# Optimization experiments

Measured on AMD Instinct MI355X. Metric: run time of the kernel, lower is better.

## Reference

```python
import jax, jax.numpy as jnp
import numpy as np


def setup_inputs() -> dict:
    key = jax.random.key(0)
    k1, k2, k3 = jax.random.split(key, 3)
    B, C, N, Ht, Wt = 2, 16, 512, 64, 64
    Ho, Wo = 1024, 1024
    x = jax.random.normal(k1, (B, C, N, Ht, Wt), dtype=jnp.float32)
    quad_idx = jax.random.randint(k2, (Ho, Wo), 0, N, dtype=jnp.int64)
    tex_uv = jax.random.uniform(k3, (Ho, Wo, 2), dtype=jnp.float32)
    return {"x": x, "quad_idx": quad_idx, "tex_uv": tex_uv}


def reference(x, quad_idx, tex_uv):
    """Per-pixel texture gather + bilinear UV sampling.

    x:        [B, C, N, Ht, Wt] atlas of N textures
    quad_idx: [Ho, Wo] int texture index per output pixel
    tex_uv:   [Ho, Wo, 2] normalized (u, v) in [0, 1]
    returns:  [B, C, Ho, Wo]
    """
    B, C, N, Ht, Wt = x.shape
    Ho, Wo = quad_idx.shape

    # map normalized uv -> pixel coordinates
    u = tex_uv[..., 0] * (Wt - 1)  # [Ho, Wo]
    v = tex_uv[..., 1] * (Ht - 1)

    x0f = jnp.floor(u)
    y0f = jnp.floor(v)
    wu = u - x0f  # bilinear weights
    wv = v - y0f

    x0 = jnp.clip(x0f.astype(jnp.int32), 0, Wt - 1)
    y0 = jnp.clip(y0f.astype(jnp.int32), 0, Ht - 1)
    x1 = jnp.clip(x0 + 1, 0, Wt - 1)
    y1 = jnp.clip(y0 + 1, 0, Ht - 1)

    # flatten texture atlas so one gather covers (texture, y, x)
    flat = x.reshape(B, C, N * Ht * Wt)
    base = quad_idx.astype(jnp.int32) * (Ht * Wt)  # [Ho, Wo]

    def gather(yi, xi):
        idx = (base + yi * Wt + xi).reshape(-1)            # [Ho*Wo]
        return jnp.take(flat, idx, axis=2).reshape(B, C, Ho, Wo)

    g00 = gather(y0, x0)
    g01 = gather(y0, x1)
    g10 = gather(y1, x0)
    g11 = gather(y1, x1)

    wu = wu[None, None]  # [1, 1, Ho, Wo]
    wv = wv[None, None]
    out = ((1.0 - wv) * ((1.0 - wu) * g00 + wu * g01)
           + wv * ((1.0 - wu) * g10 + wu * g11))
    return out
```

## Files before the change

kernel.cpp:

```cpp
#include <hip/hip_runtime.h>

#define HT 64
#define WT 64
#define NTEX 512
#define HO 1024
#define WO 1024
#define NCH 32
#define SLAB (HT * WT)
#define NPIX (HO * WO)

typedef float    f32x4 __attribute__((ext_vector_type(4)));
typedef unsigned u32x4 __attribute__((ext_vector_type(4)));

#define WS_BASE   0
#define WS_CURSOR 4096
#define WS_T1     16384
#define MB (1u << 20)
#define WS_NEED_SMALL ((size_t)WS_T1 + 8 * (size_t)MB)
#define WS_NEED_BIG   ((size_t)WS_T1 + 140 * (size_t)MB)

#define HB_PIX 4096
__global__ __launch_bounds__(256) void k_hist(const int* __restrict__ qi,
                                              unsigned* __restrict__ hist) {
    __shared__ unsigned h[NTEX];
    for (int i = threadIdx.x; i < NTEX; i += 256) h[i] = 0;
    __syncthreads();
    const int p0 = blockIdx.x * HB_PIX;
    for (int k = threadIdx.x; k < HB_PIX; k += 256)
        atomicAdd(&h[qi[p0 + k]], 1u);
    __syncthreads();
    for (int i = threadIdx.x; i < NTEX; i += 256) {
        unsigned v = h[i];
        if (v) atomicAdd(&hist[i << 4], v);
    }
}

__global__ __launch_bounds__(512) void k_scan(const unsigned* __restrict__ hist,
                                              unsigned* __restrict__ base,
                                              unsigned* __restrict__ cursor) {
    __shared__ unsigned t[NTEX];
    const int i = threadIdx.x;
    const unsigned h = hist[i << 4];
    t[i] = h;
    __syncthreads();
    for (int s = 1; s < NTEX; s <<= 1) {
        unsigned v = (i >= s) ? t[i - s] : 0u;
        __syncthreads();
        t[i] += v;
        __syncthreads();
    }
    const unsigned excl = t[i] - h;
    base[i] = excl;
    cursor[i << 2] = excl;
    if (i == NTEX - 1) base[NTEX] = t[i];
}

#define MR_PIX 4096
__global__ __launch_bounds__(256) void k_meta(const int* __restrict__ qi,
                                              const float* __restrict__ uvp,
                                              unsigned* __restrict__ cursor,
                                              uint2* __restrict__ meta,
                                              unsigned* __restrict__ rank_of) {
    __shared__ unsigned lcount[NTEX];
    __shared__ unsigned lbase[NTEX];
    const int p0 = blockIdx.x * MR_PIX;

    for (int i = threadIdx.x; i < NTEX; i += 256) lcount[i] = 0;
    __syncthreads();
    for (int k = threadIdx.x; k < MR_PIX; k += 256)
        atomicAdd(&lcount[qi[p0 + k]], 1u);
    __syncthreads();
    for (int i = threadIdx.x; i < NTEX; i += 256) {
        const unsigned cnum = lcount[i];
        lbase[i] = cnum ? atomicAdd(&cursor[i << 2], cnum) : 0u;
    }
    __syncthreads();
    for (int i = threadIdx.x; i < NTEX; i += 256) lcount[i] = 0;
    __syncthreads();

    for (int k = threadIdx.x; k < MR_PIX; k += 256) {
        const int pix = p0 + k;
        const int n = qi[pix];
        const float2 uv = reinterpret_cast<const float2*>(uvp)[pix];

        const float u = uv.x * (float)(WT - 1);
        const float v = uv.y * (float)(HT - 1);
        int x0 = (int)floorf(u);
        int y0 = (int)floorf(v);
        x0 = min(max(x0, 0), WT - 2);
        y0 = min(max(y0, 0), HT - 2);
        const float wu = u - (float)x0;
        const float wv = v - (float)y0;

        const unsigned off  = (unsigned)(y0 * WT + x0);
        const unsigned key  = ((unsigned)pix << 12) | off;
        const unsigned wu16 = (unsigned)__float2int_rn(wu * 65535.0f);
        const unsigned wv16 = (unsigned)__float2int_rn(wv * 65535.0f);

        const unsigned rank = lbase[n] + atomicAdd(&lcount[n], 1u);
        meta[rank] = make_uint2(key, wu16 | (wv16 << 16));
        if (rank_of) rank_of[pix] = rank;
    }
}

__global__ __launch_bounds__(256) void k_gather(const float* __restrict__ x,
                                                const unsigned* __restrict__ base,
                                                const uint2* __restrict__ meta,
                                                float* __restrict__ compact) {
    __shared__ float s[SLAB];

    const int b = blockIdx.x;
    const int xcd = b & 7;
    const int i = b >> 3;
    const int cgrp = i >> 9;
    const int n = i & 511;
    const int c = cgrp * 8 + xcd;

    const f32x4* __restrict__ slab4 =
        reinterpret_cast<const f32x4*>(x + ((size_t)c * NTEX + n) * SLAB);
    f32x4* s4 = reinterpret_cast<f32x4*>(s);
    #pragma unroll
    for (int j = 0; j < 4; ++j)
        s4[threadIdx.x + 256 * j] = slab4[threadIdx.x + 256 * j];
    __syncthreads();

    const unsigned lo = base[n];
    const unsigned cnt = base[n + 1] - lo;
    const uint2* __restrict__ m = meta + lo;
    float* __restrict__ cc = compact + (size_t)c * NPIX + lo;

    for (unsigned j = threadIdx.x; j < cnt; j += 256) {
        const uint2 r = m[j];
        const unsigned off = r.x & 4095u;
        const float wu = (float)(r.y & 65535u) * (1.0f / 65535.0f);
        const float wv = (float)(r.y >> 16) * (1.0f / 65535.0f);

        const float g00 = s[off];
        const float g01 = s[off + 1];
        const float g10 = s[off + WT];
        const float g11 = s[off + WT + 1];

        const float top = g00 + wu * (g01 - g00);
        const float bot = g10 + wu * (g11 - g10);
        __builtin_nontemporal_store(top + wv * (bot - top), cc + j);
    }
}

__global__ __launch_bounds__(256) void k_scatter(const unsigned* __restrict__ rank_of,
                                                 const float* __restrict__ compact,
                                                 float* __restrict__ out) {
    const int b = blockIdx.x;
    const int xcd = b & 7;
    const int q = b >> 3;
    const int cg = q >> 10;
    const int tile = q & 1023;
    const int c = cg * 8 + xcd;

    const float* __restrict__ cc = compact + (size_t)c * NPIX;
    const int p0 = tile * 1024 + threadIdx.x * 4;

    const u32x4 r = *reinterpret_cast<const u32x4*>(rank_of + p0);
    f32x4 v;
    v.x = cc[r.x];
    v.y = cc[r.y];
    v.z = cc[r.z];
    v.w = cc[r.w];
    __builtin_nontemporal_store(v,
        reinterpret_cast<f32x4*>(out + (size_t)c * NPIX + p0));
}

__global__ __launch_bounds__(256) void k_main(const float* __restrict__ x,
                                              const unsigned* __restrict__ base,
                                              const uint2* __restrict__ meta,
                                              float* __restrict__ out) {
    __shared__ float s[SLAB];

    const int b = blockIdx.x;
    const int xcd = b & 7;
    const int i = b >> 3;
    const int cgrp = i >> 9;
    const int n = i & 511;
    const int c = cgrp * 8 + xcd;

    const f32x4* __restrict__ slab4 =
        reinterpret_cast<const f32x4*>(x + ((size_t)c * NTEX + n) * SLAB);
    f32x4* s4 = reinterpret_cast<f32x4*>(s);
    #pragma unroll
    for (int j = 0; j < 4; ++j)
        s4[threadIdx.x + 256 * j] = slab4[threadIdx.x + 256 * j];
    __syncthreads();

    const unsigned lo = base[n];
    const unsigned cnt = base[n + 1] - lo;
    const uint2* __restrict__ m = meta + lo;
    float* __restrict__ o = out + (size_t)c * NPIX;

    for (unsigned j = threadIdx.x; j < cnt; j += 256) {
        const uint2 r = m[j];
        const unsigned off = r.x & 4095u;
        const unsigned pix = r.x >> 12;
        const float wu = (float)(r.y & 65535u) * (1.0f / 65535.0f);
        const float wv = (float)(r.y >> 16) * (1.0f / 65535.0f);

        const float g00 = s[off];
        const float g01 = s[off + 1];
        const float g10 = s[off + WT];
        const float g11 = s[off + WT + 1];

        const float top = g00 + wu * (g01 - g00);
        const float bot = g10 + wu * (g11 - g10);
        o[pix] = top + wv * (bot - top);
    }
}

__global__ __launch_bounds__(256) void k_direct(const float* __restrict__ x,
                                                const int* __restrict__ quad_idx,
                                                const float* __restrict__ tex_uv,
                                                float* __restrict__ out) {
    const int pix = blockIdx.x * blockDim.x + threadIdx.x;
    const int chunk = blockIdx.y;
    const int n = quad_idx[pix];
    const float2 uv = reinterpret_cast<const float2*>(tex_uv)[pix];
    const float u = uv.x * (float)(WT - 1);
    const float v = uv.y * (float)(HT - 1);
    int x0 = (int)floorf(u), y0 = (int)floorf(v);
    x0 = min(max(x0, 0), WT - 2);
    y0 = min(max(y0, 0), HT - 2);
    const float wu = u - (float)x0, wv = v - (float)y0;
    const float w00 = (1.f - wu) * (1.f - wv), w01 = wu * (1.f - wv);
    const float w10 = (1.f - wu) * wv, w11 = wu * wv;
    const int off0 = n * SLAB + y0 * WT + x0, off1 = off0 + WT;
    const float* p = x + (size_t)chunk * 8 * NTEX * SLAB;
    float* o = out + (size_t)chunk * 8 * NPIX + pix;
    #pragma unroll
    for (int ch = 0; ch < 8; ++ch) {
        float2 r0, r1;
        __builtin_memcpy(&r0, p + off0, 8);
        __builtin_memcpy(&r1, p + off1, 8);
        o[0] = w00 * r0.x + w01 * r0.y + w10 * r1.x + w11 * r1.y;
        p += (size_t)NTEX * SLAB;
        o += NPIX;
    }
}

extern "C" void kernel_launch(void* const* d_in, const int* in_sizes, int n_in,
                              void* d_out, int out_size, void* d_ws, size_t ws_size,
                              hipStream_t stream) {
    const float* x        = (const float*)d_in[0];
    const int*   quad_idx = (const int*)d_in[1];
    const float* tex_uv   = (const float*)d_in[2];
    float*       out      = (float*)d_out;
    char* ws = (char*)d_ws;

    if (ws_size >= WS_NEED_BIG) {
        unsigned* base    = (unsigned*)(ws + WS_BASE);
        unsigned* cursor  = (unsigned*)(ws + WS_CURSOR);
        unsigned* rank_of = (unsigned*)(ws + WS_T1);
        uint2*    meta    = (uint2*)(ws + WS_T1 + 4 * (size_t)MB);
        float*    compact = (float*)(ws + WS_T1 + 12 * (size_t)MB);
        unsigned* hist    = (unsigned*)(ws + WS_T1 + 12 * (size_t)MB);

        (void)hipMemsetAsync(hist, 0, NTEX * 64, stream);
        k_hist<<<NPIX / HB_PIX, 256, 0, stream>>>(quad_idx, hist);
        k_scan<<<1, 512, 0, stream>>>(hist, base, cursor);
        k_meta<<<NPIX / MR_PIX, 256, 0, stream>>>(quad_idx, tex_uv, cursor,
                                                  meta, rank_of);
        k_gather<<<NTEX * NCH, 256, 0, stream>>>(x, base, meta, compact);
        k_scatter<<<NPIX / 1024 * NCH, 256, 0, stream>>>(rank_of, compact, out);
    } else if (ws_size >= WS_NEED_SMALL) {
        unsigned* base   = (unsigned*)(ws + WS_BASE);
        unsigned* cursor = (unsigned*)(ws + WS_CURSOR);
        uint2*    meta   = (uint2*)(ws + WS_T1);
        unsigned* hist   = (unsigned*)(ws + WS_T1);

        (void)hipMemsetAsync(hist, 0, NTEX * 64, stream);
        k_hist<<<NPIX / HB_PIX, 256, 0, stream>>>(quad_idx, hist);
        k_scan<<<1, 512, 0, stream>>>(hist, base, cursor);
        k_meta<<<NPIX / MR_PIX, 256, 0, stream>>>(quad_idx, tex_uv, cursor,
                                                  meta, (unsigned*)nullptr);
        k_main<<<NTEX * NCH, 256, 0, stream>>>(x, base, meta, out);
    } else {
        dim3 grid(NPIX / 256, 4);
        k_direct<<<grid, 256, 0, stream>>>(x, quad_idx, tex_uv, out);
    }
}
```

Before: 622.5 us.

## Interleave 8 channels per compact entry and scatter all 32 channels per pixel

The gather kernel now loads 8 channel slabs (128 KB of LDS) per block and writes 8 interpolated channels per pixel as one 32-byte vector, so each meta record is read once per 8 channels instead of once per channel. The scatter kernel reads each pixel's rank once and fetches all 32 channels as 32-byte chunks from the channel-interleaved compact buffer, replacing 4 scalar random reads per thread with contiguous vector reads. The large LDS footprint limits occupancy to about one block per CU, which may reduce latency hiding during the gather.

```diff
diff --git a/kernel.cpp b/kernel.cpp
--- a/kernel.cpp
+++ b/kernel.cpp
@@ -10,7 +10,7 @@
 #define NPIX (HO * WO)
 
 typedef float    f32x4 __attribute__((ext_vector_type(4)));
-typedef unsigned u32x4 __attribute__((ext_vector_type(4)));
+typedef float    f32x8 __attribute__((ext_vector_type(8)));
 
 #define WS_BASE   0
 #define WS_CURSOR 4096
@@ -103,70 +103,73 @@
     }
 }
 
-__global__ __launch_bounds__(256) void k_gather(const float* __restrict__ x,
-                                                const unsigned* __restrict__ base,
-                                                const uint2* __restrict__ meta,
-                                                float* __restrict__ compact) {
-    __shared__ float s[SLAB];
-
+__global__ __launch_bounds__(512) void k_gather8(const float* __restrict__ x,
+                                                 const unsigned* __restrict__ base,
+                                                 const uint2* __restrict__ meta,
+                                                 float* __restrict__ compact) {
+    __shared__ float s[8 * SLAB];
     const int b = blockIdx.x;
-    const int xcd = b & 7;
-    const int i = b >> 3;
-    const int cgrp = i >> 9;
-    const int n = i & 511;
-    const int c = cgrp * 8 + xcd;
-
-    const f32x4* __restrict__ slab4 =
-        reinterpret_cast<const f32x4*>(x + ((size_t)c * NTEX + n) * SLAB);
-    f32x4* s4 = reinterpret_cast<f32x4*>(s);
-    #pragma unroll
-    for (int j = 0; j < 4; ++j)
-        s4[threadIdx.x + 256 * j] = slab4[threadIdx.x + 256 * j];
+    const int n = b & 511;
+    const int cg = b >> 9;
+    const int tid = threadIdx.x;
+
+    #pragma unroll
+    for (int ch = 0; ch < 8; ++ch) {
+        const f32x4* __restrict__ src = reinterpret_cast<const f32x4*>(
+            x + ((size_t)(cg * 8 + ch) * NTEX + n) * SLAB);
+        f32x4* d = reinterpret_cast<f32x4*>(s + ch * SLAB);
+        d[tid]       = src[tid];
+        d[tid + 512] = src[tid + 512];
+    }
     __syncthreads();
 
     const unsigned lo = base[n];
     const unsigned cnt = base[n + 1] - lo;
     const uint2* __restrict__ m = meta + lo;
-    float* __restrict__ cc = compact + (size_t)c * NPIX + lo;
-
-    for (unsigned j = threadIdx.x; j < cnt; j += 256) {
+    float* __restrict__ cc = compact + ((size_t)cg * NPIX + lo) * 8;
+
+    for (unsigned j = tid; j < cnt; j += 512) {
         const uint2 r = m[j];
         const unsigned off = r.x & 4095u;
         const float wu = (float)(r.y & 65535u) * (1.0f / 65535.0f);
         const float wv = (float)(r.y >> 16) * (1.0f / 65535.0f);
 
-        const float g00 = s[off];
-        const float g01 = s[off + 1];
-        const float g10 = s[off + WT];
-        const float g11 = s[off + WT + 1];
-
-        const float top = g00 + wu * (g01 - g00);
-        const float bot = g10 + wu * (g11 - g10);
-        __builtin_nontemporal_store(top + wv * (bot - top), cc + j);
-    }
-}
-
-__global__ __launch_bounds__(256) void k_scatter(const unsigned* __restrict__ rank_of,
-                                                 const float* __restrict__ compact,
-                                                 float* __restrict__ out) {
-    const int b = blockIdx.x;
-    const int xcd = b & 7;
-    const int q = b >> 3;
-    const int cg = q >> 10;
-    const int tile = q & 1023;
-    const int c = cg * 8 + xcd;
-
-    const float* __restrict__ cc = compact + (size_t)c * NPIX;
-    const int p0 = tile * 1024 + threadIdx.x * 4;
-
-    const u32x4 r = *reinterpret_cast<const u32x4*>(rank_of + p0);
-    f32x4 v;
-    v.x = cc[r.x];
-    v.y = cc[r.y];
-    v.z = cc[r.z];
-    v.w = cc[r.w];
-    __builtin_nontemporal_store(v,
-        reinterpret_cast<f32x4*>(out + (size_t)c * NPIX + p0));
+        f32x8 o;
+        #pragma unroll
+        for (int ch = 0; ch < 8; ++ch) {
+            const float* __restrict__ sc = s + ch * SLAB + off;
+            const float g00 = sc[0];
+            const float g01 = sc[1];
+            const float g10 = sc[WT];
+            const float g11 = sc[WT + 1];
+            const float top = g00 + wu * (g01 - g00);
+            const float bot = g10 + wu * (g11 - g10);
+            o[ch] = top + wv * (bot - top);
+        }
+        __builtin_nontemporal_store(o,
+            reinterpret_cast<f32x8*>(cc + (size_t)j * 8));
+    }
+}
+
+__global__ __launch_bounds__(256) void k_scatter32(const unsigned* __restrict__ rank_of,
+                                                   const float* __restrict__ compact,
+                                                   float* __restrict__ out) {
+    const int t = threadIdx.x;
+    const int P = blockIdx.x * 256;
+    const size_t r = (size_t)rank_of[P + t];
+
+    f32x4 v[8];
+    #pragma unroll
+    for (int cg = 0; cg < 4; ++cg) {
+        const f32x4* __restrict__ src = reinterpret_cast<const f32x4*>(
+            compact + ((size_t)cg * NPIX + r) * 8);
+        v[cg * 2]     = src[0];
+        v[cg * 2 + 1] = src[1];
+    }
+    float* __restrict__ o = out + P + t;
+    #pragma unroll
+    for (int c = 0; c < 32; ++c)
+        __builtin_nontemporal_store(v[c >> 2][c & 3], o + (size_t)c * NPIX);
 }
 
 __global__ __launch_bounds__(256) void k_main(const float* __restrict__ x,
@@ -265,8 +268,8 @@
         k_scan<<<1, 512, 0, stream>>>(hist, base, cursor);
         k_meta<<<NPIX / MR_PIX, 256, 0, stream>>>(quad_idx, tex_uv, cursor,
                                                   meta, rank_of);
-        k_gather<<<NTEX * NCH, 256, 0, stream>>>(x, base, meta, compact);
-        k_scatter<<<NPIX / 1024 * NCH, 256, 0, stream>>>(rank_of, compact, out);
+        k_gather8<<<NTEX * 4, 512, 0, stream>>>(x, base, meta, compact);
+        k_scatter32<<<NPIX / 256, 256, 0, stream>>>(rank_of, compact, out);
     } else if (ws_size >= WS_NEED_SMALL) {
         unsigned* base   = (unsigned*)(ws + WS_BASE);
         unsigned* cursor = (unsigned*)(ws + WS_CURSOR);
```

Result: faster. 554.8 us (-10.9%).
